# Performance work log

Measured on AMD Instinct MI355X. Metric: run time of the kernel, lower is better.

Reference implementation:

```python
import jax, jax.numpy as jnp
import numpy as np

N = 50000
F_IN = 128
HID = 64
HEADS = 8
E = 400000
NEG_SLOPE = 0.2
EPS = 1e-16


def setup_inputs() -> dict:
    key = jax.random.key(0)
    ks = jax.random.split(key, 10)
    x = jax.random.normal(ks[0], (N, F_IN), dtype=jnp.float32)
    edge_index = jax.random.randint(ks[1], (2, E), 0, N, dtype=jnp.int64)
    # GATConv layer 1: in=F_IN, out=HID, heads=HEADS (concat)
    s1 = 1.0 / np.sqrt(F_IN)
    W1 = jax.random.uniform(ks[2], (F_IN, HEADS * HID), jnp.float32, -s1, s1)
    a_src1 = jax.random.uniform(ks[3], (HEADS, HID), jnp.float32, -s1, s1)
    a_dst1 = jax.random.uniform(ks[4], (HEADS, HID), jnp.float32, -s1, s1)
    b1 = jnp.zeros((HEADS * HID,), jnp.float32)
    # GATConv layer 2: in=HEADS*HID, out=2, heads=1
    s2 = 1.0 / np.sqrt(HEADS * HID)
    W2 = jax.random.uniform(ks[5], (HEADS * HID, 1 * 2), jnp.float32, -s2, s2)
    a_src2 = jax.random.uniform(ks[6], (1, 2), jnp.float32, -s2, s2)
    a_dst2 = jax.random.uniform(ks[7], (1, 2), jnp.float32, -s2, s2)
    b2 = jnp.zeros((2,), jnp.float32)
    return {"x": x, "edge_index": edge_index, "W1": W1, "a_src1": a_src1,
            "a_dst1": a_dst1, "b1": b1, "W2": W2, "a_src2": a_src2,
            "a_dst2": a_dst2, "b2": b2}


def gat_conv(x, src, dst, W, a_src, a_dst, bias, heads, out_ch):
    n = x.shape[0]
    h = (x @ W).reshape(n, heads, out_ch)              # [N,H,C]
    alpha_s = jnp.einsum('nhc,hc->nh', h, a_src)       # [N,H]
    alpha_d = jnp.einsum('nhc,hc->nh', h, a_dst)
    e = jax.nn.leaky_relu(alpha_s[src] + alpha_d[dst], NEG_SLOPE)  # [E,H]
    # scatter-softmax over incoming edges per destination node
    e_max = jax.ops.segment_max(e, dst, num_segments=n)
    e_exp = jnp.exp(e - e_max[dst])
    denom = jax.ops.segment_sum(e_exp, dst, num_segments=n)
    alpha = e_exp / (denom[dst] + EPS)                 # [E,H]
    msg = alpha[:, :, None] * h[src]                   # [E,H,C]
    out = jax.ops.segment_sum(msg, dst, num_segments=n)
    return out.reshape(n, heads * out_ch) + bias


def reference(x, edge_index, W1, a_src1, a_dst1, b1, W2, a_src2, a_dst2, b2):
    n = x.shape[0]
    loops = jnp.arange(n, dtype=edge_index.dtype)
    src = jnp.concatenate([edge_index[0], loops])      # PyG adds self-loops
    dst = jnp.concatenate([edge_index[1], loops])
    h = gat_conv(x, src, dst, W1, a_src1, a_dst1, b1, HEADS, HID)
    h = jax.nn.relu(h)
    # F.dropout(p=0.5, training=self.training): identity in eval mode
    out = gat_conv(h, src, dst, W2, a_src2, a_dst2, b2, 1, 2)
    return out
```

## Files before the change

### kernel.cpp

```cpp
#include <hip/hip_runtime.h>
#include <hip/hip_bf16.h>

#define NN 50000
#define NE 400000
#define NET (NE + NN)
#define F1 512
#define SLOPE 0.2f
#define GEPS 1e-16f
#define BCAP 64

#define GEMM_BLKS 391
#define SCAT_BLKS ((NET + 255) / 256)

typedef __attribute__((ext_vector_type(8))) short bf16x8;
typedef __attribute__((ext_vector_type(4))) short bf16x4;
typedef __attribute__((ext_vector_type(4))) float f32x4;
typedef __attribute__((ext_vector_type(2))) float f32x2;

#define SWZ(b) ((b) ^ ((((b) >> 8) & 7) << 4))

static __device__ __forceinline__ unsigned short f2b(float f) {
  __hip_bfloat16 b = __float2bfloat16(f);
  return __builtin_bit_cast(unsigned short, b);
}
static __device__ __forceinline__ float bitsf(unsigned u) {
  return __builtin_bit_cast(float, u);
}

__global__ __launch_bounds__(256) void prep_k(const float* __restrict__ W,
                                              unsigned short* __restrict__ wt) {
  const int i = blockIdx.x * 256 + threadIdx.x;
  if (i < F1 * 128) {
    const int n = i >> 7, k = i & 127;
    wt[i] = f2b(W[k * F1 + n]);
  }
}

__global__ __launch_bounds__(256) void gemm_scat_k(const float* __restrict__ x,
                                                   const unsigned short* __restrict__ wt,
                                                   const float* __restrict__ a_src,
                                                   const float* __restrict__ a_dst,
                                                   __hip_bfloat16* __restrict__ h,
                                                   float* __restrict__ as1,
                                                   float* __restrict__ ad1,
                                                   const int* __restrict__ ei,
                                                   int* __restrict__ cnt,
                                                   int* __restrict__ csr) {
  const int t = threadIdx.x;

  if (blockIdx.x >= GEMM_BLKS) {
    const int e = (blockIdx.x - GEMM_BLKS) * 256 + t;
    if (e >= NET) return;
    int s, d;
    if (e < NE) { s = ei[e]; d = ei[NE + e]; }
    else        { s = e - NE; d = s; }
    if ((unsigned)d >= NN || (unsigned)s >= NN) return;
    const int pos = atomicAdd(&cnt[d], 1);
    if (pos < BCAP) csr[d * BCAP + pos] = s;
    return;
  }

  __shared__ char lds[65536];
  const int m0 = blockIdx.x * 128;
  const int l16 = t & 15, g16 = t >> 4;

#pragma unroll
  for (int p = 0; p < 8; ++p) {
    const int row = p * 16 + g16;
    const int gm = m0 + row;
    bf16x8 av = {};
    if (gm < NN) {
      const float4 f0 = *(const float4*)(x + (size_t)gm * 128 + l16 * 8);
      const float4 f1 = *(const float4*)(x + (size_t)gm * 128 + l16 * 8 + 4);
      av[0] = f2b(f0.x); av[1] = f2b(f0.y); av[2] = f2b(f0.z); av[3] = f2b(f0.w);
      av[4] = f2b(f1.x); av[5] = f2b(f1.y); av[6] = f2b(f1.z); av[7] = f2b(f1.w);
    }
    *(bf16x8*)(lds + SWZ(row * 256 + l16 * 16)) = av;
  }

  const int w = t >> 6;
  const int lane = t & 63;
  const int lrow = lane & 15;
  const int kgrp = (lane >> 4) * 8;
  const int rbase = (lane >> 4) * 4;

  for (int nt = 0; nt < 4; ++nt) {
    const int n0 = nt * 128;
#pragma unroll
    for (int p = 0; p < 8; ++p) {
      const int row = p * 16 + g16;
      const bf16x8 bv = *(const bf16x8*)(wt + (size_t)(n0 + row) * 128 + l16 * 8);
      *(bf16x8*)(lds + 32768 + SWZ(row * 256 + l16 * 16)) = bv;
    }
    __syncthreads();

    f32x4 acc[2][8] = {};
#pragma unroll
    for (int ks = 0; ks < 4; ++ks) {
      const int kb = (ks * 32 + kgrp) * 2;
      bf16x8 a[2], b[8];
#pragma unroll
      for (int mr = 0; mr < 2; ++mr) {
        const int row = w * 32 + mr * 16 + lrow;
        a[mr] = *(const bf16x8*)(lds + SWZ(row * 256 + kb));
      }
#pragma unroll
      for (int nr = 0; nr < 8; ++nr) {
        const int rowb = nr * 16 + lrow;
        b[nr] = *(const bf16x8*)(lds + 32768 + SWZ(rowb * 256 + kb));
      }
#pragma unroll
      for (int mr = 0; mr < 2; ++mr)
#pragma unroll
        for (int nr = 0; nr < 8; ++nr)
          acc[mr][nr] = __builtin_amdgcn_mfma_f32_16x16x32_bf16(a[mr], b[nr], acc[mr][nr], 0, 0, 0);
    }

    const int head0 = n0 >> 6;
    float asv[8], adv[8];
#pragma unroll
    for (int nr = 0; nr < 8; ++nr) {
      const int cwh = (nr & 3) * 16 + lrow;
      asv[nr] = a_src[(head0 + (nr >> 2)) * 64 + cwh];
      adv[nr] = a_dst[(head0 + (nr >> 2)) * 64 + cwh];
    }
#pragma unroll
    for (int mr = 0; mr < 2; ++mr) {
#pragma unroll
      for (int r = 0; r < 4; ++r) {
        const int grow = m0 + w * 32 + mr * 16 + rbase + r;
        if (grow >= NN) continue;
        float s0 = 0.f, s1 = 0.f, d0 = 0.f, d1 = 0.f;
#pragma unroll
        for (int nr = 0; nr < 8; ++nr) {
          const float v = acc[mr][nr][r];
          h[(size_t)grow * F1 + n0 + nr * 16 + lrow] = __float2bfloat16(v);
          if (nr < 4) { s0 = fmaf(v, asv[nr], s0); d0 = fmaf(v, adv[nr], d0); }
          else        { s1 = fmaf(v, asv[nr], s1); d1 = fmaf(v, adv[nr], d1); }
        }
#pragma unroll
        for (int m = 1; m < 16; m <<= 1) {
          s0 += __shfl_xor(s0, m); s1 += __shfl_xor(s1, m);
          d0 += __shfl_xor(d0, m); d1 += __shfl_xor(d1, m);
        }
        if (lrow == 0) {
          as1[grow * 8 + head0] = s0; as1[grow * 8 + head0 + 1] = s1;
          ad1[grow * 8 + head0] = d0; ad1[grow * 8 + head0 + 1] = d1;
        }
      }
    }
    if (nt < 3) __syncthreads();
  }
}

__global__ __launch_bounds__(256) void agg1_k(const __hip_bfloat16* __restrict__ h,
                                              const float* __restrict__ as1,
                                              const float* __restrict__ ad1,
                                              const float* __restrict__ b1,
                                              const int* __restrict__ cnt,
                                              const int* __restrict__ csr,
                                              const float* __restrict__ W2,
                                              const float* __restrict__ a_s2,
                                              const float* __restrict__ a_d2,
                                              float* __restrict__ g,
                                              float* __restrict__ s2,
                                              float* __restrict__ d2) {
  __shared__ float pg[4][2];
  const int t = threadIdx.x;
  const int w = t >> 6;
  const int lane = t & 63;
  const int node = blockIdx.x * 2 + (w >> 1);
  const int half = w & 1;
  const int head = half * 4 + (lane >> 4);
  const unsigned choff = (unsigned)(half * 256 + lane * 4);

  const float adv = ad1[node * 8 + head];
  int degn = cnt[node];
  degn = (degn > BCAP) ? BCAP : degn;
  const int cbase = node * BCAP;
  const unsigned short* hp = (const unsigned short*)h;

  f32x2 acc2[2] = {};
  float den = 0.f;

#define LOADC(ss, hh, aa)                                              \
  hh = *(const bf16x4*)(hp + (unsigned)(ss) * (unsigned)F1 + choff);   \
  aa = as1[(ss) * 8 + head];

#define CONSUME(hh, aa)                                                \
  {                                                                    \
    float ev = (aa) + adv;                                             \
    ev = (ev > 0.f) ? ev : ev * SLOPE;                                 \
    const float pe = __expf(ev);                                       \
    den += pe;                                                         \
    const f32x2 pv = {pe, pe};                                         \
    const unsigned* hu = (const unsigned*)&(hh);                       \
    _Pragma("unroll")                                                  \
    for (int i = 0; i < 2; ++i) {                                      \
      const unsigned u = hu[i];                                        \
      const f32x2 hv2 = {bitsf(u << 16), bitsf(u & 0xffff0000u)};      \
      acc2[i] = __builtin_elementwise_fma(pv, hv2, acc2[i]);           \
    }                                                                  \
  }

  int idx = 0;
  const bool have = (idx + 4 <= degn);
  bf16x4 hA = {}, hB = {}, hC = {}, hD = {};
  float aA = 0.f, aB = 0.f, aC = 0.f, aD = 0.f;
  if (have) {
    const int cA = csr[cbase], cB = csr[cbase + 1], cC = csr[cbase + 2], cD = csr[cbase + 3];
    LOADC(cA, hA, aA); LOADC(cB, hB, aB); LOADC(cC, hC, aC); LOADC(cD, hD, aD);
  }
  for (; idx + 8 <= degn; idx += 4) {
    const int nA = csr[cbase + idx + 4], nB = csr[cbase + idx + 5];
    const int nC = csr[cbase + idx + 6], nD = csr[cbase + idx + 7];
    bf16x4 xA, xB, xC, xD;
    float yA, yB, yC, yD;
    LOADC(nA, xA, yA); LOADC(nB, xB, yB); LOADC(nC, xC, yC); LOADC(nD, xD, yD);
    CONSUME(hA, aA); CONSUME(hB, aB); CONSUME(hC, aC); CONSUME(hD, aD);
    hA = xA; hB = xB; hC = xC; hD = xD;
    aA = yA; aB = yB; aC = yC; aD = yD;
  }
  if (have) {
    CONSUME(hA, aA); CONSUME(hB, aB); CONSUME(hC, aC); CONSUME(hD, aD);
    idx += 4;
  }
  for (; idx < degn; ++idx) {
    const int s = csr[cbase + idx];
    bf16x4 hv; float av;
    LOADC(s, hv, av);
    CONSUME(hv, av);
  }
#undef LOADC
#undef CONSUME

  const float inv = 1.f / (den + GEPS);
  float g0 = 0.f, g1 = 0.f;
#pragma unroll
  for (int i = 0; i < 2; ++i) {
#pragma unroll
    for (int k = 0; k < 2; ++k) {
      const int c = half * 256 + lane * 4 + 2 * i + k;
      const float v = fmaxf(fmaf(k ? acc2[i].y : acc2[i].x, inv, b1[c]), 0.f);
      g0 = fmaf(v, W2[2 * c + 0], g0);
      g1 = fmaf(v, W2[2 * c + 1], g1);
    }
  }
#pragma unroll
  for (int m = 1; m < 64; m <<= 1) {
    g0 += __shfl_xor(g0, m);
    g1 += __shfl_xor(g1, m);
  }
  if (lane == 0) { pg[w][0] = g0; pg[w][1] = g1; }
  __syncthreads();
  if (half == 0 && lane == 0) {
    const float G0 = pg[w][0] + pg[w + 1][0];
    const float G1 = pg[w][1] + pg[w + 1][1];
    g[node * 2 + 0] = G0;
    g[node * 2 + 1] = G1;
    s2[node] = G0 * a_s2[0] + G1 * a_s2[1];
    d2[node] = G0 * a_d2[0] + G1 * a_d2[1];
  }
}

__global__ __launch_bounds__(256) void agg2_k(const float* __restrict__ g,
                                              const float* __restrict__ s2,
                                              const float* __restrict__ d2,
                                              const float* __restrict__ b2,
                                              const int* __restrict__ cnt,
                                              const int* __restrict__ csr,
                                              float* __restrict__ out) {
  const int gid = blockIdx.x * 256 + threadIdx.x;
  const int node = gid >> 3;
  if (node >= NN) return;
  const int sub = threadIdx.x & 7;
  const float adv = d2[node];
  int degn = cnt[node];
  degn = (degn > BCAP) ? BCAP : degn;
  const int cbase = node * BCAP;
  float den = 0.f, a0 = 0.f, a1 = 0.f;
  int idx = sub;
  for (; idx + 8 < degn; idx += 16) {
    const int sA = csr[cbase + idx];
    const int sB = csr[cbase + idx + 8];
    const float2 gA = *(const float2*)(g + 2 * sA);
    const float2 gB = *(const float2*)(g + 2 * sB);
    float eA = s2[sA] + adv; eA = (eA > 0.f) ? eA : eA * SLOPE;
    float eB = s2[sB] + adv; eB = (eB > 0.f) ? eB : eB * SLOPE;
    const float pA = __expf(eA);
    const float pB = __expf(eB);
    den += pA + pB;
    a0 = fmaf(pA, gA.x, a0); a1 = fmaf(pA, gA.y, a1);
    a0 = fmaf(pB, gB.x, a0); a1 = fmaf(pB, gB.y, a1);
  }
  if (idx < degn) {
    const int s = csr[cbase + idx];
    const float2 gv = *(const float2*)(g + 2 * s);
    float ev = s2[s] + adv;
    ev = (ev > 0.f) ? ev : ev * SLOPE;
    const float p = __expf(ev);
    den += p;
    a0 = fmaf(p, gv.x, a0); a1 = fmaf(p, gv.y, a1);
  }
#pragma unroll
  for (int m = 1; m < 8; m <<= 1) {
    den += __shfl_xor(den, m);
    a0 += __shfl_xor(a0, m);
    a1 += __shfl_xor(a1, m);
  }
  if (sub == 0) {
    const float inv = 1.f / (den + GEPS);
    out[2 * node + 0] = a0 * inv + b2[0];
    out[2 * node + 1] = a1 * inv + b2[1];
  }
}

extern "C" void kernel_launch(void* const* d_in, const int* in_sizes, int n_in,
                              void* d_out, int out_size, void* d_ws, size_t ws_size,
                              hipStream_t stream) {
  (void)in_sizes; (void)n_in; (void)out_size; (void)ws_size;
  const float* x = (const float*)d_in[0];
  const int* ei = (const int*)d_in[1];
  const float* W1 = (const float*)d_in[2];
  const float* a_src1 = (const float*)d_in[3];
  const float* a_dst1 = (const float*)d_in[4];
  const float* b1 = (const float*)d_in[5];
  const float* W2 = (const float*)d_in[6];
  const float* a_src2 = (const float*)d_in[7];
  const float* a_dst2 = (const float*)d_in[8];
  const float* b2 = (const float*)d_in[9];
  float* out = (float*)d_out;

  char* ws = (char*)d_ws;
  auto alloc = [&](size_t bytes) { char* p = ws; ws += (bytes + 255) & ~(size_t)255; return p; };
  __hip_bfloat16* h = (__hip_bfloat16*)alloc((size_t)NN * F1 * 2);
  unsigned short* wt = (unsigned short*)alloc((size_t)F1 * 128 * 2);
  float* as1 = (float*)alloc((size_t)NN * 8 * 4);
  float* ad1 = (float*)alloc((size_t)NN * 8 * 4);
  int* cnt = (int*)alloc((size_t)NN * 4);
  int* csr = (int*)alloc((size_t)NN * BCAP * 4);
  float* g = (float*)alloc((size_t)NN * 2 * 4);
  float* s2 = (float*)alloc((size_t)NN * 4);
  float* d2 = (float*)alloc((size_t)NN * 4);

  hipMemsetAsync(cnt, 0, (size_t)NN * 4, stream);

  prep_k<<<(F1 * 128 + 255) / 256, 256, 0, stream>>>(W1, wt);
  gemm_scat_k<<<GEMM_BLKS + SCAT_BLKS, 256, 0, stream>>>(x, wt, a_src1, a_dst1, h, as1, ad1,
                                                         ei, cnt, csr);
  agg1_k<<<NN / 2, 256, 0, stream>>>(h, as1, ad1, b1, cnt, csr, W2, a_src2, a_dst2, g, s2, d2);
  agg2_k<<<(NN * 8 + 255) / 256, 256, 0, stream>>>(g, s2, d2, b2, cnt, csr, out);
}
```

Before: 124.8 us.

## Map one wavefront per node in layer-1 aggregation with 16-byte gathers

Each node in the first aggregation kernel is now handled by a single 64-lane wavefront instead of two. Each lane loads 8 bf16 channels (16 bytes) per neighbor rather than 4. This removes the shared-memory partial sums and the block-wide barrier, and halves the redundant per-wave loads of the CSR indices and attention scalars. The costs are more accumulator registers per lane and half as many wavefronts in flight to hide gather latency.

```diff
diff --git a/kernel.cpp b/kernel.cpp
--- a/kernel.cpp
+++ b/kernel.cpp
@@ -13,7 +13,6 @@
 #define SCAT_BLKS ((NET + 255) / 256)
 
 typedef __attribute__((ext_vector_type(8))) short bf16x8;
-typedef __attribute__((ext_vector_type(4))) short bf16x4;
 typedef __attribute__((ext_vector_type(4))) float f32x4;
 typedef __attribute__((ext_vector_type(2))) float f32x2;
 
@@ -165,26 +164,23 @@
                                               float* __restrict__ g,
                                               float* __restrict__ s2,
                                               float* __restrict__ d2) {
-  __shared__ float pg[4][2];
-  const int t = threadIdx.x;
-  const int w = t >> 6;
-  const int lane = t & 63;
-  const int node = blockIdx.x * 2 + (w >> 1);
-  const int half = w & 1;
-  const int head = half * 4 + (lane >> 4);
-  const unsigned choff = (unsigned)(half * 256 + lane * 4);
-
+  const int gid = blockIdx.x * 256 + threadIdx.x;
+  const int node = __builtin_amdgcn_readfirstlane(gid >> 6);
+  if (node >= NN) return;
+  const int lane = threadIdx.x & 63;
+  const int head = lane >> 3;
   const float adv = ad1[node * 8 + head];
   int degn = cnt[node];
   degn = (degn > BCAP) ? BCAP : degn;
   const int cbase = node * BCAP;
   const unsigned short* hp = (const unsigned short*)h;
-
-  f32x2 acc2[2] = {};
+  const unsigned loff = (unsigned)(lane * 8);
+
+  f32x2 acc2[4] = {};
   float den = 0.f;
 
 #define LOADC(ss, hh, aa)                                              \
-  hh = *(const bf16x4*)(hp + (unsigned)(ss) * (unsigned)F1 + choff);   \
+  hh = *(const bf16x8*)(hp + (unsigned)(ss) * (unsigned)F1 + loff);    \
   aa = as1[(ss) * 8 + head];
 
 #define CONSUME(hh, aa)                                                \
@@ -196,7 +192,7 @@
     const f32x2 pv = {pe, pe};                                         \
     const unsigned* hu = (const unsigned*)&(hh);                       \
     _Pragma("unroll")                                                  \
-    for (int i = 0; i < 2; ++i) {                                      \
+    for (int i = 0; i < 4; ++i) {                                      \
       const unsigned u = hu[i];                                        \
       const f32x2 hv2 = {bitsf(u << 16), bitsf(u & 0xffff0000u)};      \
       acc2[i] = __builtin_elementwise_fma(pv, hv2, acc2[i]);           \
@@ -205,7 +201,7 @@
 
   int idx = 0;
   const bool have = (idx + 4 <= degn);
-  bf16x4 hA = {}, hB = {}, hC = {}, hD = {};
+  bf16x8 hA = {}, hB = {}, hC = {}, hD = {};
   float aA = 0.f, aB = 0.f, aC = 0.f, aD = 0.f;
   if (have) {
     const int cA = csr[cbase], cB = csr[cbase + 1], cC = csr[cbase + 2], cD = csr[cbase + 3];
@@ -214,7 +210,7 @@
   for (; idx + 8 <= degn; idx += 4) {
     const int nA = csr[cbase + idx + 4], nB = csr[cbase + idx + 5];
     const int nC = csr[cbase + idx + 6], nD = csr[cbase + idx + 7];
-    bf16x4 xA, xB, xC, xD;
+    bf16x8 xA, xB, xC, xD;
     float yA, yB, yC, yD;
     LOADC(nA, xA, yA); LOADC(nB, xB, yB); LOADC(nC, xC, yC); LOADC(nD, xD, yD);
     CONSUME(hA, aA); CONSUME(hB, aB); CONSUME(hC, aC); CONSUME(hD, aD);
@@ -227,7 +223,7 @@
   }
   for (; idx < degn; ++idx) {
     const int s = csr[cbase + idx];
-    bf16x4 hv; float av;
+    bf16x8 hv; float av;
     LOADC(s, hv, av);
     CONSUME(hv, av);
   }
@@ -237,10 +233,10 @@
   const float inv = 1.f / (den + GEPS);
   float g0 = 0.f, g1 = 0.f;
 #pragma unroll
-  for (int i = 0; i < 2; ++i) {
+  for (int i = 0; i < 4; ++i) {
 #pragma unroll
     for (int k = 0; k < 2; ++k) {
-      const int c = half * 256 + lane * 4 + 2 * i + k;
+      const int c = lane * 8 + 2 * i + k;
       const float v = fmaxf(fmaf(k ? acc2[i].y : acc2[i].x, inv, b1[c]), 0.f);
       g0 = fmaf(v, W2[2 * c + 0], g0);
       g1 = fmaf(v, W2[2 * c + 1], g1);
@@ -251,15 +247,11 @@
     g0 += __shfl_xor(g0, m);
     g1 += __shfl_xor(g1, m);
   }
-  if (lane == 0) { pg[w][0] = g0; pg[w][1] = g1; }
-  __syncthreads();
-  if (half == 0 && lane == 0) {
-    const float G0 = pg[w][0] + pg[w + 1][0];
-    const float G1 = pg[w][1] + pg[w + 1][1];
-    g[node * 2 + 0] = G0;
-    g[node * 2 + 1] = G1;
-    s2[node] = G0 * a_s2[0] + G1 * a_s2[1];
-    d2[node] = G0 * a_d2[0] + G1 * a_d2[1];
+  if (lane == 0) {
+    g[node * 2 + 0] = g0;
+    g[node * 2 + 1] = g1;
+    s2[node] = g0 * a_s2[0] + g1 * a_s2[1];
+    d2[node] = g0 * a_d2[0] + g1 * a_d2[1];
   }
 }
 
@@ -348,6 +340,6 @@
   prep_k<<<(F1 * 128 + 255) / 256, 256, 0, stream>>>(W1, wt);
   gemm_scat_k<<<GEMM_BLKS + SCAT_BLKS, 256, 0, stream>>>(x, wt, a_src1, a_dst1, h, as1, ad1,
                                                          ei, cnt, csr);
-  agg1_k<<<NN / 2, 256, 0, stream>>>(h, as1, ad1, b1, cnt, csr, W2, a_src2, a_dst2, g, s2, d2);
+  agg1_k<<<(NN * 64) / 256, 256, 0, stream>>>(h, as1, ad1, b1, cnt, csr, W2, a_src2, a_dst2, g, s2, d2);
   agg2_k<<<(NN * 8 + 255) / 256, 256, 0, stream>>>(g, s2, d2, b2, cnt, csr, out);
 }
```

After: 117.1 us. -6.2%, faster.
